# Kernel tuning notes

Hardware: AMD Instinct MI355X
Metric: run time of the kernel (lower is better)

Reference implementation:

```python
import jax, jax.numpy as jnp
import numpy as np

B, H, S, DH = 2, 16, 2048, 64
MASK_FILL = -10000.0


def setup_inputs() -> dict:
    key = jax.random.key(0)
    kq, kk, kv = jax.random.split(key, 3)
    q = jax.random.normal(kq, (B, H, S, DH), dtype=jnp.float32)
    k = jax.random.normal(kk, (B, H, S, DH), dtype=jnp.float32)
    v = jax.random.normal(kv, (B, H, S, DH), dtype=jnp.float32)
    # causal mask: True where attention is disallowed (upper triangle)
    mask = jnp.triu(jnp.ones((S, S), dtype=jnp.bool_), k=1)
    return {"q": q, "k": k, "v": v, "mask": mask}


def reference(q, k, v, mask):
    scale = 1.0 / jnp.sqrt(jnp.asarray(k.shape[-1], dtype=q.dtype))
    # scores: [B, H, S_q, S_k]
    scores = jnp.einsum("bhqd,bhkd->bhqk", q, k) * scale
    # additive mask: masked_fill on a zeros [S_k, S_v] matrix -> -10000 where mask
    attn_bias = jnp.where(mask, jnp.asarray(MASK_FILL, dtype=k.dtype),
                          jnp.asarray(0.0, dtype=k.dtype))
    scores = scores + attn_bias  # broadcast over batch/heads
    attn = jax.nn.softmax(scores, axis=-1)
    # dropout_rate = 0.0 -> identity
    return jnp.einsum("bhqk,bhkd->bhqd", attn, v)
```

## Files before the change

kernel.cpp:

```cpp
#include <hip/hip_runtime.h>


#define S_LEN  2048
#define DHDIM  64
#define NHEADS 32
#define LDP    72
#define M2     23.083120654223414f
#define QSCALE 0.18033688011117658f
#define NSLOT  27

typedef __attribute__((ext_vector_type(8))) short bf16x8;
typedef __attribute__((ext_vector_type(4))) float f32x4;
typedef __attribute__((ext_vector_type(16))) float f32x16;

#define RT(qp,k0,k1,sl) ((unsigned)(qp)<<24 | (unsigned)(k0)<<16 | (unsigned)(k1)<<8 | (unsigned)(sl))
__device__ __constant__ unsigned RTAB32[32] = {
    RT(15,0,11,24),  RT(15,11,22,25), RT(10,0,11,10),  RT(10,11,22,11),
    RT(15,22,32,26), RT(14,0,10,21),  RT(14,10,20,22), RT(14,20,30,23),
    RT(13,0,10,18),  RT(9,0,10,8),    RT(9,10,20,9),   RT(4,0,10,255),
    RT(13,10,19,19), RT(13,19,28,20), RT(12,0,9,15),   RT(12,9,18,16),
    RT(8,0,9,6),     RT(8,9,18,7),    RT(12,18,26,17), RT(11,0,8,12),
    RT(11,8,16,13),  RT(11,16,24,14), RT(7,0,8,4),     RT(7,8,16,5),
    RT(3,0,8,255),   RT(6,0,7,2),     RT(6,7,14,3),    RT(5,0,6,0),
    RT(5,6,12,1),    RT(2,0,6,255),   RT(1,0,4,255),   RT(0,0,2,255)};

__device__ __forceinline__ float fast_exp2(float x) {
#if __has_builtin(__builtin_amdgcn_exp2f)
    return __builtin_amdgcn_exp2f(x);
#else
    return exp2f(x);
#endif
}
__device__ __forceinline__ unsigned short f2bf(float f) {
    unsigned u = __float_as_uint(f);
    return (unsigned short)((u + 0x7fffu + ((u >> 16) & 1u)) >> 16);
}
__device__ __forceinline__ void ld8(const float* p, float* f) {
    float4 a = *(const float4*)p, b = *(const float4*)(p + 4);
    f[0]=a.x; f[1]=a.y; f[2]=a.z; f[3]=a.w; f[4]=b.x; f[5]=b.y; f[6]=b.z; f[7]=b.w;
}
__device__ __forceinline__ uint4 pack8(const float* f, float scale) {
    union { uint4 v; unsigned short s[8]; } w;
    #pragma unroll
    for (int j = 0; j < 8; j++) w.s[j] = f2bf(f[j] * scale);
    return w.v;
}
__device__ __forceinline__ unsigned packhi(float a, float b) {
#if __has_builtin(__builtin_amdgcn_perm)
    return __builtin_amdgcn_perm(__float_as_uint(b), __float_as_uint(a), 0x07060302u);
#else
    return (__float_as_uint(a) >> 16) | (__float_as_uint(b) & 0xffff0000u);
#endif
}
__device__ __forceinline__ bf16x8 mk_bf16x8(unsigned d0, unsigned d1,
                                            unsigned d2, unsigned d3) {
    union { unsigned u[4]; bf16x8 v; } w;
    w.u[0] = d0; w.u[1] = d1; w.u[2] = d2; w.u[3] = d3;
    return w.v;
}

__global__ __launch_bounds__(256) void prep(
    const float* __restrict__ Qf, const float* __restrict__ Kf,
    const float* __restrict__ Vf, unsigned short* __restrict__ qb,
    unsigned short* __restrict__ kb, unsigned short* __restrict__ vtb)
{
    const int st = blockIdx.x, bh = blockIdx.y;
    __shared__ unsigned lt32[64][LDP / 2];
    const float* vp = Vf + ((size_t)bh * S_LEN + st * 64) * DHDIM;
    {
        const int c = threadIdx.x;
        const int sp = c >> 3;
        const int d0 = (c & 7) * 8;
        float fa[8], fb[8];
        ld8(vp + (2 * sp) * DHDIM + d0, fa);
        ld8(vp + (2 * sp + 1) * DHDIM + d0, fb);
        #pragma unroll
        for (int j = 0; j < 8; j++) {
            int d = d0 + j;
            int colw = (sp & 3) | ((((sp >> 2) ^ (d >> 3)) & 7) << 2);
            lt32[d][colw] = (unsigned)f2bf(fa[j]) | ((unsigned)f2bf(fb[j]) << 16);
        }
    }
    size_t off = ((size_t)(bh * 32 + st) * 4096) + (size_t)threadIdx.x * 16;
    float f[8];
    ld8(Qf + off, f);     *(uint4*)(qb + off)     = pack8(f, QSCALE);
    ld8(Qf + off + 8, f); *(uint4*)(qb + off + 8) = pack8(f, QSCALE);
    ld8(Kf + off, f);     *(uint4*)(kb + off)     = pack8(f, 1.0f);
    ld8(Kf + off + 8, f); *(uint4*)(kb + off + 8) = pack8(f, 1.0f);
    __syncthreads();
    unsigned short* op = vtb + (size_t)bh * DHDIM * S_LEN + st * 64;
    for (int c = threadIdx.x; c < 512; c += 256) {
        int d = c >> 3, q = c & 7;
        int colw = ((q ^ (d >> 3)) & 7) << 2;
        *(uint4*)(op + (size_t)d * S_LEN + q * 8) = *(const uint4*)&lt32[d][colw];
    }
}

__global__ __launch_bounds__(512) void fattn_splitk(
    const unsigned short* __restrict__ Qp, const unsigned short* __restrict__ Kp,
    const unsigned short* __restrict__ Vp,
    float* __restrict__ pO, float* __restrict__ pL, float* __restrict__ O)
{
    __shared__ unsigned short smem[256 * LDP];
    unsigned short (*ksA)[LDP]  = (unsigned short(*)[LDP])smem;
    unsigned short (*ksB)[LDP]  = (unsigned short(*)[LDP])(smem + 64 * LDP);
    unsigned short (*vtsA)[LDP] = (unsigned short(*)[LDP])(smem + 128 * LDP);
    unsigned short (*vtsB)[LDP] = (unsigned short(*)[LDP])(smem + 192 * LDP);

    const int bh   = blockIdx.x;
    const unsigned e = RTAB32[blockIdx.y];
    const int qp   = e >> 24;
    const int k0   = (e >> 16) & 255;
    const int k1   = (e >> 8) & 255;
    const int sl   = e & 255;
    const bool whole = (sl == 255);

    const int tid  = threadIdx.x;
    const int wave = tid >> 6, lane = tid & 63;
    const int q31  = lane & 31, hi = lane >> 5;
    const int qh   = wave & 3, kh = wave >> 2;
    const int qrow = qh * 32 + q31;
    const int gq   = qp * 128 + qrow;
    const int diag_kt = gq >> 6;

    const unsigned short* qsrc = Qp + ((size_t)bh * S_LEN + gq) * DHDIM;
    const bf16x8 bq0 = *(const bf16x8*)(qsrc + hi * 8);
    const bf16x8 bq1 = *(const bf16x8*)(qsrc + 16 + hi * 8);
    const bf16x8 bq2 = *(const bf16x8*)(qsrc + 32 + hi * 8);
    const bf16x8 bq3 = *(const bf16x8*)(qsrc + 48 + hi * 8);

    f32x16 of2[2];
    #pragma unroll
    for (int i = 0; i < 16; i++) { of2[0][i] = 0.f; of2[1][i] = 0.f; }
    float l_p = 0.f;

    const unsigned short* Kbh = Kp + (size_t)bh * S_LEN * DHDIM;
    const unsigned short* Vbh = Vp + (size_t)bh * DHDIM * S_LEN;
    const int sr = tid >> 3, sc = (tid & 7) * 8;
    uint4 kr, vr;
    kr = *(const uint4*)(Kbh + ((size_t)k0 * 64 + sr) * DHDIM + sc);
    vr = *(const uint4*)(Vbh + (size_t)sr * S_LEN + k0 * 64 + sc);
    {
        unsigned short (*ks)[LDP]  = (k0 & 1) ? ksB : ksA;
        unsigned short (*vts)[LDP] = (k0 & 1) ? vtsB : vtsA;
        *(uint4*)&ks[sr][sc]  = kr;
        *(uint4*)&vts[sr][sc] = vr;
    }
    if (k0 + 1 < k1) {
        kr = *(const uint4*)(Kbh + ((size_t)(k0 + 1) * 64 + sr) * DHDIM + sc);
        vr = *(const uint4*)(Vbh + (size_t)sr * S_LEN + (k0 + 1) * 64 + sc);
    }

    for (int kt = k0; kt < k1; kt++) {
        __syncthreads();

        if (kt + 1 < k1) {
            unsigned short (*ks)[LDP]  = ((kt + 1) & 1) ? ksB : ksA;
            unsigned short (*vts)[LDP] = ((kt + 1) & 1) ? vtsB : vtsA;
            *(uint4*)&ks[sr][sc]  = kr;
            *(uint4*)&vts[sr][sc] = vr;
            if (kt + 2 < k1) {
                kr = *(const uint4*)(Kbh + ((size_t)(kt + 2) * 64 + sr) * DHDIM + sc);
                vr = *(const uint4*)(Vbh + (size_t)sr * S_LEN + (kt + 2) * 64 + sc);
            }
        }

        if (kt > diag_kt) continue;

        const unsigned short (*ksc)[LDP] = (kt & 1) ? ksB : ksA;
        const unsigned short (*vtc)[LDP] = (kt & 1) ? vtsB : vtsA;

        f32x16 sf;
        #pragma unroll
        for (int i = 0; i < 16; i++) sf[i] = -M2;
        __builtin_amdgcn_s_setprio(1);
        {
            bf16x8 ak = *(const bf16x8*)&ksc[kh * 32 + q31][hi * 8];
            sf = __builtin_amdgcn_mfma_f32_32x32x16_bf16(ak, bq0, sf, 0, 0, 0);
            ak = *(const bf16x8*)&ksc[kh * 32 + q31][16 + hi * 8];
            sf = __builtin_amdgcn_mfma_f32_32x32x16_bf16(ak, bq1, sf, 0, 0, 0);
            ak = *(const bf16x8*)&ksc[kh * 32 + q31][32 + hi * 8];
            sf = __builtin_amdgcn_mfma_f32_32x32x16_bf16(ak, bq2, sf, 0, 0, 0);
            ak = *(const bf16x8*)&ksc[kh * 32 + q31][48 + hi * 8];
            sf = __builtin_amdgcn_mfma_f32_32x32x16_bf16(ak, bq3, sf, 0, 0, 0);
        }
        __builtin_amdgcn_s_setprio(0);

        const bool diag = (kt == diag_kt);
        const int qmod = gq & 63;
        unsigned pdw[8];
        #pragma unroll
        for (int g = 0; g < 4; g++) {
            float p[4];
            #pragma unroll
            for (int r2 = 0; r2 < 4; r2++) {
                float pv = fast_exp2(sf[g * 4 + r2]);
                if (diag) {
                    const int kl = kh * 32 + 8 * g + 4 * hi + r2;
                    if (kl > qmod) pv = 0.f;
                }
                p[r2] = pv;
                l_p += pv;
            }
            pdw[g * 2]     = packhi(p[0], p[1]);
            pdw[g * 2 + 1] = packhi(p[2], p[3]);
        }

        __builtin_amdgcn_s_setprio(1);
        #pragma unroll
        for (int js = 0; js < 2; js++) {
            const unsigned a0 = pdw[4 * js],     a1 = pdw[4 * js + 1];
            const unsigned b0 = pdw[4 * js + 2], b1 = pdw[4 * js + 3];
            const unsigned pa0 = __shfl_xor(a0, 32), pa1 = __shfl_xor(a1, 32);
            const unsigned pb0 = __shfl_xor(b0, 32), pb1 = __shfl_xor(b1, 32);
            const bf16x8 bp = mk_bf16x8(hi ? pb0 : a0, hi ? pb1 : a1,
                                        hi ? b0 : pa0, hi ? b1 : pa1);
            const int scol = (2 * kh + js) * 16 + hi * 8;
            bf16x8 av = *(const bf16x8*)&vtc[q31][scol];
            of2[0] = __builtin_amdgcn_mfma_f32_32x32x16_bf16(av, bp, of2[0], 0, 0, 0);
            av = *(const bf16x8*)&vtc[32 + q31][scol];
            of2[1] = __builtin_amdgcn_mfma_f32_32x32x16_bf16(av, bp, of2[1], 0, 0, 0);
        }
        __builtin_amdgcn_s_setprio(0);
    }

    float l2 = l_p + __shfl_xor(l_p, 32);
    __syncthreads();
    float* fs = (float*)smem;
    const int base = (qh * 64 + lane) * 36;
    if (kh == 1) {
        #pragma unroll
        for (int dh = 0; dh < 2; dh++)
            #pragma unroll
            for (int g = 0; g < 4; g++)
                *(float4*)&fs[base + dh * 16 + g * 4] = make_float4(
                    of2[dh][4 * g], of2[dh][4 * g + 1],
                    of2[dh][4 * g + 2], of2[dh][4 * g + 3]);
        fs[base + 32] = l2;
    }
    __syncthreads();
    if (kh == 0) {
        #pragma unroll
        for (int dh = 0; dh < 2; dh++)
            #pragma unroll
            for (int g = 0; g < 4; g++) {
                float4 a = *(const float4*)&fs[base + dh * 16 + g * 4];
                of2[dh][4 * g]     += a.x;
                of2[dh][4 * g + 1] += a.y;
                of2[dh][4 * g + 2] += a.z;
                of2[dh][4 * g + 3] += a.w;
            }
        l2 += fs[base + 32];

        if (whole) {
            const float inv = 1.f / l2;
            float* op = O + ((size_t)bh * S_LEN + gq) * DHDIM;
            #pragma unroll
            for (int dh = 0; dh < 2; dh++)
                #pragma unroll
                for (int g = 0; g < 4; g++)
                    *(float4*)(op + dh * 32 + 8 * g + 4 * hi) = make_float4(
                        of2[dh][4 * g] * inv, of2[dh][4 * g + 1] * inv,
                        of2[dh][4 * g + 2] * inv, of2[dh][4 * g + 3] * inv);
        } else {
            const int slot = bh * NSLOT + sl;
            if (hi == 0) pL[slot * 128 + qrow] = l2;
            float* op = pO + (size_t)slot * 8192 + qrow * 64;
            #pragma unroll
            for (int dh = 0; dh < 2; dh++)
                #pragma unroll
                for (int g = 0; g < 4; g++)
                    *(float4*)(op + dh * 32 + 8 * g + 4 * hi) = make_float4(
                        of2[dh][4 * g], of2[dh][4 * g + 1],
                        of2[dh][4 * g + 2], of2[dh][4 * g + 3]);
        }
    }
}

__global__ __launch_bounds__(256) void combine(
    const float* __restrict__ pO, const float* __restrict__ pL,
    float* __restrict__ O)
{
    const int t = 5 + blockIdx.x, bh = blockIdx.y;
    int base, cnt;
    if (t <= 10) { base = (t - 5) * 2;       cnt = 2; }
    else         { base = 12 + (t - 11) * 3; cnt = 3; }
    const int sb = bh * NSLOT + base;
    const float* A = pO + (size_t)sb * 8192;
    float* out = O + ((size_t)bh * S_LEN + t * 128) * DHDIM;
    #pragma unroll
    for (int k = 0; k < 8; k++) {
        int c = threadIdx.x + k * 256;
        int row = c >> 4;
        float l = pL[sb * 128 + row] + pL[(sb + 1) * 128 + row];
        float4 a = *(const float4*)(A + c * 4);
        float4 b = *(const float4*)(A + 8192 + c * 4);
        float4 s = make_float4(a.x + b.x, a.y + b.y, a.z + b.z, a.w + b.w);
        if (cnt == 3) {
            l += pL[(sb + 2) * 128 + row];
            float4 d = *(const float4*)(A + 16384 + c * 4);
            s = make_float4(s.x + d.x, s.y + d.y, s.z + d.z, s.w + d.w);
        }
        float inv = 1.f / l;
        *(float4*)(out + c * 4) = make_float4(
            s.x * inv, s.y * inv, s.z * inv, s.w * inv);
    }
}

template <bool PRE>
__global__ __launch_bounds__(256) void fattn_kernel(
    const void* __restrict__ Qp, const void* __restrict__ Kp,
    const void* __restrict__ Vp, float* __restrict__ O)
{
    __shared__ unsigned short smem[192 * LDP];
    unsigned short (*ks)[LDP]  = (unsigned short(*)[LDP])smem;
    unsigned short (*vts)[LDP] = (unsigned short(*)[LDP])(smem + 64 * LDP);
    unsigned short (*qs)[LDP]  = (unsigned short(*)[LDP])(smem + 128 * LDP);
    unsigned short (*pst)[LDP] = qs;

    const int id = blockIdx.y * 32 + blockIdx.x;
    const int g  = id >> 8;
    const int r8 = id & 255;
    const int bh = r8 >> 3;
    const int s8 = r8 & 7;
    const int qt = (g == 0) ? 31 - 2 * s8 : (g == 1) ? 2 * s8
                 : (g == 2) ? 30 - 2 * s8 : 2 * s8 + 1;

    const int tid = threadIdx.x;
    const int wave = tid >> 6, lane = tid & 63;
    const int quad = lane >> 4, l16 = lane & 15;

    if constexpr (PRE) {
        const unsigned short* src = (const unsigned short*)Qp
            + ((size_t)bh * S_LEN + qt * 64) * DHDIM;
        for (int c = tid; c < 512; c += 256) {
            int row = c >> 3, c8 = (c & 7) * 8;
            *(uint4*)&qs[row][c8] = *(const uint4*)(src + row * DHDIM + c8);
        }
    } else {
        const float* src = (const float*)Qp + ((size_t)bh * S_LEN + qt * 64) * DHDIM;
        for (int c = tid; c < 512; c += 256) {
            int row = c >> 3, c8 = (c & 7) * 8;
            float f[8]; ld8(src + row * DHDIM + c8, f);
            *(uint4*)&qs[row][c8] = pack8(f, QSCALE);
        }
    }
    __syncthreads();

    const int prow = wave * 16 + l16;
    const bf16x8 bq0 = *(const bf16x8*)&qs[prow][quad * 8];
    const bf16x8 bq1 = *(const bf16x8*)&qs[prow][32 + quad * 8];

    float l_p = 0.f;
    f32x4 of[4];
    #pragma unroll
    for (int n = 0; n < 4; n++) of[n] = (f32x4){0.f, 0.f, 0.f, 0.f};

    for (int kt = 0; kt <= qt; kt++) {
        __syncthreads();
        if constexpr (PRE) {
            const unsigned short* ksrc = (const unsigned short*)Kp
                + ((size_t)bh * S_LEN + kt * 64) * DHDIM;
            const unsigned short* vsrc = (const unsigned short*)Vp
                + (size_t)bh * DHDIM * S_LEN + kt * 64;
            for (int c = tid; c < 512; c += 256) {
                int row = c >> 3, c8 = (c & 7) * 8;
                *(uint4*)&ks[row][c8]  = *(const uint4*)(ksrc + row * DHDIM + c8);
                *(uint4*)&vts[row][c8] = *(const uint4*)(vsrc + (size_t)row * S_LEN + c8);
            }
        } else {
            const float* ksrc = (const float*)Kp + ((size_t)bh * S_LEN + kt * 64) * DHDIM;
            const float* vsrc = (const float*)Vp + ((size_t)bh * S_LEN + kt * 64) * DHDIM;
            for (int c = tid; c < 512; c += 256) {
                int row = c >> 3, c8 = (c & 7) * 8;
                float f[8];
                ld8(ksrc + row * DHDIM + c8, f);
                *(uint4*)&ks[row][c8] = pack8(f, 1.0f);
                ld8(vsrc + row * DHDIM + c8, f);
                #pragma unroll
                for (int j = 0; j < 8; j++) vts[c8 + j][row] = f2bf(f[j]);
            }
        }
        __syncthreads();

        f32x4 sf[4];
        #pragma unroll
        for (int n = 0; n < 4; n++) {
            bf16x8 ak0 = *(const bf16x8*)&ks[n * 16 + l16][quad * 8];
            bf16x8 ak1 = *(const bf16x8*)&ks[n * 16 + l16][32 + quad * 8];
            sf[n] = (f32x4){-M2, -M2, -M2, -M2};
            sf[n] = __builtin_amdgcn_mfma_f32_16x16x32_bf16(ak0, bq0, sf[n], 0, 0, 0);
            sf[n] = __builtin_amdgcn_mfma_f32_16x16x32_bf16(ak1, bq1, sf[n], 0, 0, 0);
        }

        const bool diag = (kt == qt);
        #pragma unroll
        for (int n = 0; n < 4; n++) {
            float p[4];
            #pragma unroll
            for (int r = 0; r < 4; r++) {
                p[r] = fast_exp2(sf[n][r]);
                if (diag && (n * 16 + quad * 4 + r > prow)) p[r] = 0.f;
                l_p += p[r];
            }
            uint2 dw;
            dw.x = packhi(p[0], p[1]);
            dw.y = packhi(p[2], p[3]);
            *(uint2*)&pst[prow][n * 16 + quad * 4] = dw;
        }
        asm volatile("s_waitcnt lgkmcnt(0)" ::: "memory");

        bf16x8 bp0 = *(const bf16x8*)&pst[prow][quad * 8];
        bf16x8 bp1 = *(const bf16x8*)&pst[prow][32 + quad * 8];
        #pragma unroll
        for (int n = 0; n < 4; n++) {
            bf16x8 av0 = *(const bf16x8*)&vts[n * 16 + l16][quad * 8];
            bf16x8 av1 = *(const bf16x8*)&vts[n * 16 + l16][32 + quad * 8];
            of[n] = __builtin_amdgcn_mfma_f32_16x16x32_bf16(av0, bp0, of[n], 0, 0, 0);
            of[n] = __builtin_amdgcn_mfma_f32_16x16x32_bf16(av1, bp1, of[n], 0, 0, 0);
        }
    }

    l_p += __shfl_xor(l_p, 16);
    l_p += __shfl_xor(l_p, 32);
    const float inv = 1.f / l_p;
    float* op = O + ((size_t)bh * S_LEN + qt * 64 + prow) * DHDIM;
    #pragma unroll
    for (int n = 0; n < 4; n++)
        *(float4*)(op + n * 16 + quad * 4) = make_float4(
            of[n][0] * inv, of[n][1] * inv, of[n][2] * inv, of[n][3] * inv);
}

extern "C" void kernel_launch(void* const* d_in, const int* in_sizes, int n_in,
                              void* d_out, int out_size, void* d_ws, size_t ws_size,
                              hipStream_t stream) {
    const float* Q = (const float*)d_in[0];
    const float* K = (const float*)d_in[1];
    const float* V = (const float*)d_in[2];
    float* O = (float*)d_out;
    const size_t N = (size_t)NHEADS * S_LEN * DHDIM;
    const size_t prepB  = 3 * N * sizeof(unsigned short);
    const size_t partB  = (size_t)NSLOT * 32 * (8192 + 128) * sizeof(float);

    if (d_ws && ws_size >= prepB + partB) {
        unsigned short* qb  = (unsigned short*)d_ws;
        unsigned short* kb  = qb + N;
        unsigned short* vtb = kb + N;
        float* pO = (float*)((char*)d_ws + prepB);
        float* pL = pO + (size_t)NSLOT * 32 * 8192;
        prep<<<dim3(S_LEN / 64, NHEADS), 256, 0, stream>>>(Q, K, V, qb, kb, vtb);
        fattn_splitk<<<dim3(32, 32), 512, 0, stream>>>(qb, kb, vtb, pO, pL, O);
        combine<<<dim3(11, 32), 256, 0, stream>>>(pO, pL, O);
    } else if (d_ws && ws_size >= prepB) {
        unsigned short* qb  = (unsigned short*)d_ws;
        unsigned short* kb  = qb + N;
        unsigned short* vtb = kb + N;
        prep<<<dim3(S_LEN / 64, NHEADS), 256, 0, stream>>>(Q, K, V, qb, kb, vtb);
        fattn_kernel<true><<<dim3(32, 32), 256, 0, stream>>>(qb, kb, vtb, O);
    } else {
        fattn_kernel<false><<<dim3(32, 32), 256, 0, stream>>>(Q, K, V, O);
    }
}
```

Before: 139.0 us.

## Replace split-K attention plus combine with paired causal q-tile blocks

Drops the split-K flash attention kernel, its partial-output workspace and the separate combine kernel. Each of 256 blocks now handles two 128-row query tiles of one head, one long (15-i) and one short (i), so causal work is balanced across blocks without partial sums. This removes the combine launch and the global traffic for partial results. In exchange the grid shrinks from 1024 blocks to 256, which may underfill the GPU's compute units, and each block processes its two tiles one after the other.

```diff
diff --git a/kernel.cpp b/kernel.cpp
--- a/kernel.cpp
+++ b/kernel.cpp
@@ -7,22 +7,10 @@
 #define LDP    72
 #define M2     23.083120654223414f
 #define QSCALE 0.18033688011117658f
-#define NSLOT  27
 
 typedef __attribute__((ext_vector_type(8))) short bf16x8;
 typedef __attribute__((ext_vector_type(4))) float f32x4;
 typedef __attribute__((ext_vector_type(16))) float f32x16;
-
-#define RT(qp,k0,k1,sl) ((unsigned)(qp)<<24 | (unsigned)(k0)<<16 | (unsigned)(k1)<<8 | (unsigned)(sl))
-__device__ __constant__ unsigned RTAB32[32] = {
-    RT(15,0,11,24),  RT(15,11,22,25), RT(10,0,11,10),  RT(10,11,22,11),
-    RT(15,22,32,26), RT(14,0,10,21),  RT(14,10,20,22), RT(14,20,30,23),
-    RT(13,0,10,18),  RT(9,0,10,8),    RT(9,10,20,9),   RT(4,0,10,255),
-    RT(13,10,19,19), RT(13,19,28,20), RT(12,0,9,15),   RT(12,9,18,16),
-    RT(8,0,9,6),     RT(8,9,18,7),    RT(12,18,26,17), RT(11,0,8,12),
-    RT(11,8,16,13),  RT(11,16,24,14), RT(7,0,8,4),     RT(7,8,16,5),
-    RT(3,0,8,255),   RT(6,0,7,2),     RT(6,7,14,3),    RT(5,0,6,0),
-    RT(5,6,12,1),    RT(2,0,6,255),   RT(1,0,4,255),   RT(0,0,2,255)};
 
 __device__ __forceinline__ float fast_exp2(float x) {
 #if __has_builtin(__builtin_amdgcn_exp2f)
@@ -96,10 +84,9 @@
     }
 }
 
-__global__ __launch_bounds__(512) void fattn_splitk(
+__global__ __launch_bounds__(512) void fattn_single(
     const unsigned short* __restrict__ Qp, const unsigned short* __restrict__ Kp,
-    const unsigned short* __restrict__ Vp,
-    float* __restrict__ pO, float* __restrict__ pL, float* __restrict__ O)
+    const unsigned short* __restrict__ Vp, float* __restrict__ O)
 {
     __shared__ unsigned short smem[256 * LDP];
     unsigned short (*ksA)[LDP]  = (unsigned short(*)[LDP])smem;
@@ -107,152 +94,150 @@
     unsigned short (*vtsA)[LDP] = (unsigned short(*)[LDP])(smem + 128 * LDP);
     unsigned short (*vtsB)[LDP] = (unsigned short(*)[LDP])(smem + 192 * LDP);
 
-    const int bh   = blockIdx.x;
-    const unsigned e = RTAB32[blockIdx.y];
-    const int qp   = e >> 24;
-    const int k0   = (e >> 16) & 255;
-    const int k1   = (e >> 8) & 255;
-    const int sl   = e & 255;
-    const bool whole = (sl == 255);
+    const int b  = blockIdx.x;
+    const int bh = b >> 3, i8 = b & 7;
 
     const int tid  = threadIdx.x;
     const int wave = tid >> 6, lane = tid & 63;
     const int q31  = lane & 31, hi = lane >> 5;
     const int qh   = wave & 3, kh = wave >> 2;
     const int qrow = qh * 32 + q31;
-    const int gq   = qp * 128 + qrow;
-    const int diag_kt = gq >> 6;
-
-    const unsigned short* qsrc = Qp + ((size_t)bh * S_LEN + gq) * DHDIM;
-    const bf16x8 bq0 = *(const bf16x8*)(qsrc + hi * 8);
-    const bf16x8 bq1 = *(const bf16x8*)(qsrc + 16 + hi * 8);
-    const bf16x8 bq2 = *(const bf16x8*)(qsrc + 32 + hi * 8);
-    const bf16x8 bq3 = *(const bf16x8*)(qsrc + 48 + hi * 8);
-
-    f32x16 of2[2];
-    #pragma unroll
-    for (int i = 0; i < 16; i++) { of2[0][i] = 0.f; of2[1][i] = 0.f; }
-    float l_p = 0.f;
 
     const unsigned short* Kbh = Kp + (size_t)bh * S_LEN * DHDIM;
     const unsigned short* Vbh = Vp + (size_t)bh * DHDIM * S_LEN;
     const int sr = tid >> 3, sc = (tid & 7) * 8;
-    uint4 kr, vr;
-    kr = *(const uint4*)(Kbh + ((size_t)k0 * 64 + sr) * DHDIM + sc);
-    vr = *(const uint4*)(Vbh + (size_t)sr * S_LEN + k0 * 64 + sc);
-    {
-        unsigned short (*ks)[LDP]  = (k0 & 1) ? ksB : ksA;
-        unsigned short (*vts)[LDP] = (k0 & 1) ? vtsB : vtsA;
-        *(uint4*)&ks[sr][sc]  = kr;
-        *(uint4*)&vts[sr][sc] = vr;
-    }
-    if (k0 + 1 < k1) {
-        kr = *(const uint4*)(Kbh + ((size_t)(k0 + 1) * 64 + sr) * DHDIM + sc);
-        vr = *(const uint4*)(Vbh + (size_t)sr * S_LEN + (k0 + 1) * 64 + sc);
-    }
-
-    for (int kt = k0; kt < k1; kt++) {
-        __syncthreads();
-
-        if (kt + 1 < k1) {
-            unsigned short (*ks)[LDP]  = ((kt + 1) & 1) ? ksB : ksA;
-            unsigned short (*vts)[LDP] = ((kt + 1) & 1) ? vtsB : vtsA;
-            *(uint4*)&ks[sr][sc]  = kr;
-            *(uint4*)&vts[sr][sc] = vr;
-            if (kt + 2 < k1) {
-                kr = *(const uint4*)(Kbh + ((size_t)(kt + 2) * 64 + sr) * DHDIM + sc);
-                vr = *(const uint4*)(Vbh + (size_t)sr * S_LEN + (kt + 2) * 64 + sc);
-            }
-        }
-
-        if (kt > diag_kt) continue;
-
-        const unsigned short (*ksc)[LDP] = (kt & 1) ? ksB : ksA;
-        const unsigned short (*vtc)[LDP] = (kt & 1) ? vtsB : vtsA;
-
-        f32x16 sf;
-        #pragma unroll
-        for (int i = 0; i < 16; i++) sf[i] = -M2;
-        __builtin_amdgcn_s_setprio(1);
-        {
-            bf16x8 ak = *(const bf16x8*)&ksc[kh * 32 + q31][hi * 8];
-            sf = __builtin_amdgcn_mfma_f32_32x32x16_bf16(ak, bq0, sf, 0, 0, 0);
-            ak = *(const bf16x8*)&ksc[kh * 32 + q31][16 + hi * 8];
-            sf = __builtin_amdgcn_mfma_f32_32x32x16_bf16(ak, bq1, sf, 0, 0, 0);
-            ak = *(const bf16x8*)&ksc[kh * 32 + q31][32 + hi * 8];
-            sf = __builtin_amdgcn_mfma_f32_32x32x16_bf16(ak, bq2, sf, 0, 0, 0);
-            ak = *(const bf16x8*)&ksc[kh * 32 + q31][48 + hi * 8];
-            sf = __builtin_amdgcn_mfma_f32_32x32x16_bf16(ak, bq3, sf, 0, 0, 0);
-        }
-        __builtin_amdgcn_s_setprio(0);
-
-        const bool diag = (kt == diag_kt);
-        const int qmod = gq & 63;
-        unsigned pdw[8];
-        #pragma unroll
-        for (int g = 0; g < 4; g++) {
-            float p[4];
-            #pragma unroll
-            for (int r2 = 0; r2 < 4; r2++) {
-                float pv = fast_exp2(sf[g * 4 + r2]);
-                if (diag) {
-                    const int kl = kh * 32 + 8 * g + 4 * hi + r2;
-                    if (kl > qmod) pv = 0.f;
+
+    #pragma unroll 1
+    for (int it = 0; it < 2; ++it) {
+        const int qp = it ? i8 : (15 - i8);
+        const int k1 = 2 * qp + 2;
+        const int gq = qp * 128 + qrow;
+        const int diag_kt = gq >> 6;
+
+        const unsigned short* qsrc = Qp + ((size_t)bh * S_LEN + gq) * DHDIM;
+        const bf16x8 bq0 = *(const bf16x8*)(qsrc + hi * 8);
+        const bf16x8 bq1 = *(const bf16x8*)(qsrc + 16 + hi * 8);
+        const bf16x8 bq2 = *(const bf16x8*)(qsrc + 32 + hi * 8);
+        const bf16x8 bq3 = *(const bf16x8*)(qsrc + 48 + hi * 8);
+
+        f32x16 of2[2];
+        #pragma unroll
+        for (int i = 0; i < 16; i++) { of2[0][i] = 0.f; of2[1][i] = 0.f; }
+        float l_p = 0.f;
+
+        __syncthreads();
+
+        uint4 kr, vr;
+        kr = *(const uint4*)(Kbh + (size_t)sr * DHDIM + sc);
+        vr = *(const uint4*)(Vbh + (size_t)sr * S_LEN + sc);
+        *(uint4*)&ksA[sr][sc]  = kr;
+        *(uint4*)&vtsA[sr][sc] = vr;
+        if (1 < k1) {
+            kr = *(const uint4*)(Kbh + ((size_t)64 + sr) * DHDIM + sc);
+            vr = *(const uint4*)(Vbh + (size_t)sr * S_LEN + 64 + sc);
+        }
+
+        for (int kt = 0; kt < k1; kt++) {
+            __syncthreads();
+
+            if (kt + 1 < k1) {
+                unsigned short (*ks)[LDP]  = ((kt + 1) & 1) ? ksB : ksA;
+                unsigned short (*vts)[LDP] = ((kt + 1) & 1) ? vtsB : vtsA;
+                *(uint4*)&ks[sr][sc]  = kr;
+                *(uint4*)&vts[sr][sc] = vr;
+                if (kt + 2 < k1) {
+                    kr = *(const uint4*)(Kbh + ((size_t)(kt + 2) * 64 + sr) * DHDIM + sc);
+                    vr = *(const uint4*)(Vbh + (size_t)sr * S_LEN + (kt + 2) * 64 + sc);
                 }
-                p[r2] = pv;
-                l_p += pv;
-            }
-            pdw[g * 2]     = packhi(p[0], p[1]);
-            pdw[g * 2 + 1] = packhi(p[2], p[3]);
-        }
-
-        __builtin_amdgcn_s_setprio(1);
-        #pragma unroll
-        for (int js = 0; js < 2; js++) {
-            const unsigned a0 = pdw[4 * js],     a1 = pdw[4 * js + 1];
-            const unsigned b0 = pdw[4 * js + 2], b1 = pdw[4 * js + 3];
-            const unsigned pa0 = __shfl_xor(a0, 32), pa1 = __shfl_xor(a1, 32);
-            const unsigned pb0 = __shfl_xor(b0, 32), pb1 = __shfl_xor(b1, 32);
-            const bf16x8 bp = mk_bf16x8(hi ? pb0 : a0, hi ? pb1 : a1,
-                                        hi ? b0 : pa0, hi ? b1 : pa1);
-            const int scol = (2 * kh + js) * 16 + hi * 8;
-            bf16x8 av = *(const bf16x8*)&vtc[q31][scol];
-            of2[0] = __builtin_amdgcn_mfma_f32_32x32x16_bf16(av, bp, of2[0], 0, 0, 0);
-            av = *(const bf16x8*)&vtc[32 + q31][scol];
-            of2[1] = __builtin_amdgcn_mfma_f32_32x32x16_bf16(av, bp, of2[1], 0, 0, 0);
-        }
-        __builtin_amdgcn_s_setprio(0);
-    }
-
-    float l2 = l_p + __shfl_xor(l_p, 32);
-    __syncthreads();
-    float* fs = (float*)smem;
-    const int base = (qh * 64 + lane) * 36;
-    if (kh == 1) {
-        #pragma unroll
-        for (int dh = 0; dh < 2; dh++)
-            #pragma unroll
-            for (int g = 0; g < 4; g++)
-                *(float4*)&fs[base + dh * 16 + g * 4] = make_float4(
-                    of2[dh][4 * g], of2[dh][4 * g + 1],
-                    of2[dh][4 * g + 2], of2[dh][4 * g + 3]);
-        fs[base + 32] = l2;
-    }
-    __syncthreads();
-    if (kh == 0) {
-        #pragma unroll
-        for (int dh = 0; dh < 2; dh++)
+            }
+
+            if (kt > diag_kt) continue;
+
+            const unsigned short (*ksc)[LDP] = (kt & 1) ? ksB : ksA;
+            const unsigned short (*vtc)[LDP] = (kt & 1) ? vtsB : vtsA;
+
+            f32x16 sf;
+            #pragma unroll
+            for (int i = 0; i < 16; i++) sf[i] = -M2;
+            __builtin_amdgcn_s_setprio(1);
+            {
+                bf16x8 ak = *(const bf16x8*)&ksc[kh * 32 + q31][hi * 8];
+                sf = __builtin_amdgcn_mfma_f32_32x32x16_bf16(ak, bq0, sf, 0, 0, 0);
+                ak = *(const bf16x8*)&ksc[kh * 32 + q31][16 + hi * 8];
+                sf = __builtin_amdgcn_mfma_f32_32x32x16_bf16(ak, bq1, sf, 0, 0, 0);
+                ak = *(const bf16x8*)&ksc[kh * 32 + q31][32 + hi * 8];
+                sf = __builtin_amdgcn_mfma_f32_32x32x16_bf16(ak, bq2, sf, 0, 0, 0);
+                ak = *(const bf16x8*)&ksc[kh * 32 + q31][48 + hi * 8];
+                sf = __builtin_amdgcn_mfma_f32_32x32x16_bf16(ak, bq3, sf, 0, 0, 0);
+            }
+            __builtin_amdgcn_s_setprio(0);
+
+            const bool diag = (kt == diag_kt);
+            const int qmod = gq & 63;
+            unsigned pdw[8];
             #pragma unroll
             for (int g = 0; g < 4; g++) {
-                float4 a = *(const float4*)&fs[base + dh * 16 + g * 4];
-                of2[dh][4 * g]     += a.x;
-                of2[dh][4 * g + 1] += a.y;
-                of2[dh][4 * g + 2] += a.z;
-                of2[dh][4 * g + 3] += a.w;
-            }
-        l2 += fs[base + 32];
-
-        if (whole) {
+                float p[4];
+                #pragma unroll
+                for (int r2 = 0; r2 < 4; r2++) {
+                    float pv = fast_exp2(sf[g * 4 + r2]);
+                    if (diag) {
+                        const int kl = kh * 32 + 8 * g + 4 * hi + r2;
+                        if (kl > qmod) pv = 0.f;
+                    }
+                    p[r2] = pv;
+                    l_p += pv;
+                }
+                pdw[g * 2]     = packhi(p[0], p[1]);
+                pdw[g * 2 + 1] = packhi(p[2], p[3]);
+            }
+
+            __builtin_amdgcn_s_setprio(1);
+            #pragma unroll
+            for (int js = 0; js < 2; js++) {
+                const unsigned a0 = pdw[4 * js],     a1 = pdw[4 * js + 1];
+                const unsigned b0 = pdw[4 * js + 2], b1 = pdw[4 * js + 3];
+                const unsigned pa0 = __shfl_xor(a0, 32), pa1 = __shfl_xor(a1, 32);
+                const unsigned pb0 = __shfl_xor(b0, 32), pb1 = __shfl_xor(b1, 32);
+                const bf16x8 bp = mk_bf16x8(hi ? pb0 : a0, hi ? pb1 : a1,
+                                            hi ? b0 : pa0, hi ? b1 : pa1);
+                const int scol = (2 * kh + js) * 16 + hi * 8;
+                bf16x8 av = *(const bf16x8*)&vtc[q31][scol];
+                of2[0] = __builtin_amdgcn_mfma_f32_32x32x16_bf16(av, bp, of2[0], 0, 0, 0);
+                av = *(const bf16x8*)&vtc[32 + q31][scol];
+                of2[1] = __builtin_amdgcn_mfma_f32_32x32x16_bf16(av, bp, of2[1], 0, 0, 0);
+            }
+            __builtin_amdgcn_s_setprio(0);
+        }
+
+        float l2 = l_p + __shfl_xor(l_p, 32);
+        __syncthreads();
+        float* fs = (float*)smem;
+        const int base = (qh * 64 + lane) * 36;
+        if (kh == 1) {
+            #pragma unroll
+            for (int dh = 0; dh < 2; dh++)
+                #pragma unroll
+                for (int g = 0; g < 4; g++)
+                    *(float4*)&fs[base + dh * 16 + g * 4] = make_float4(
+                        of2[dh][4 * g], of2[dh][4 * g + 1],
+                        of2[dh][4 * g + 2], of2[dh][4 * g + 3]);
+            fs[base + 32] = l2;
+        }
+        __syncthreads();
+        if (kh == 0) {
+            #pragma unroll
+            for (int dh = 0; dh < 2; dh++)
+                #pragma unroll
+                for (int g = 0; g < 4; g++) {
+                    float4 a = *(const float4*)&fs[base + dh * 16 + g * 4];
+                    of2[dh][4 * g]     += a.x;
+                    of2[dh][4 * g + 1] += a.y;
+                    of2[dh][4 * g + 2] += a.z;
+                    of2[dh][4 * g + 3] += a.w;
+                }
+            l2 += fs[base + 32];
+
             const float inv = 1.f / l2;
             float* op = O + ((size_t)bh * S_LEN + gq) * DHDIM;
             #pragma unroll
@@ -262,48 +247,7 @@
                     *(float4*)(op + dh * 32 + 8 * g + 4 * hi) = make_float4(
                         of2[dh][4 * g] * inv, of2[dh][4 * g + 1] * inv,
                         of2[dh][4 * g + 2] * inv, of2[dh][4 * g + 3] * inv);
-        } else {
-            const int slot = bh * NSLOT + sl;
-            if (hi == 0) pL[slot * 128 + qrow] = l2;
-            float* op = pO + (size_t)slot * 8192 + qrow * 64;
-            #pragma unroll
-            for (int dh = 0; dh < 2; dh++)
-                #pragma unroll
-                for (int g = 0; g < 4; g++)
-                    *(float4*)(op + dh * 32 + 8 * g + 4 * hi) = make_float4(
-                        of2[dh][4 * g], of2[dh][4 * g + 1],
-                        of2[dh][4 * g + 2], of2[dh][4 * g + 3]);
-        }
-    }
-}
-
-__global__ __launch_bounds__(256) void combine(
-    const float* __restrict__ pO, const float* __restrict__ pL,
-    float* __restrict__ O)
-{
-    const int t = 5 + blockIdx.x, bh = blockIdx.y;
-    int base, cnt;
-    if (t <= 10) { base = (t - 5) * 2;       cnt = 2; }
-    else         { base = 12 + (t - 11) * 3; cnt = 3; }
-    const int sb = bh * NSLOT + base;
-    const float* A = pO + (size_t)sb * 8192;
-    float* out = O + ((size_t)bh * S_LEN + t * 128) * DHDIM;
-    #pragma unroll
-    for (int k = 0; k < 8; k++) {
-        int c = threadIdx.x + k * 256;
-        int row = c >> 4;
-        float l = pL[sb * 128 + row] + pL[(sb + 1) * 128 + row];
-        float4 a = *(const float4*)(A + c * 4);
-        float4 b = *(const float4*)(A + 8192 + c * 4);
-        float4 s = make_float4(a.x + b.x, a.y + b.y, a.z + b.z, a.w + b.w);
-        if (cnt == 3) {
-            l += pL[(sb + 2) * 128 + row];
-            float4 d = *(const float4*)(A + 16384 + c * 4);
-            s = make_float4(s.x + d.x, s.y + d.y, s.z + d.z, s.w + d.w);
-        }
-        float inv = 1.f / l;
-        *(float4*)(out + c * 4) = make_float4(
-            s.x * inv, s.y * inv, s.z * inv, s.w * inv);
+        }
     }
 }
 
@@ -440,23 +384,13 @@
     float* O = (float*)d_out;
     const size_t N = (size_t)NHEADS * S_LEN * DHDIM;
     const size_t prepB  = 3 * N * sizeof(unsigned short);
-    const size_t partB  = (size_t)NSLOT * 32 * (8192 + 128) * sizeof(float);
-
-    if (d_ws && ws_size >= prepB + partB) {
-        unsigned short* qb  = (unsigned short*)d_ws;
-        unsigned short* kb  = qb + N;
-        unsigned short* vtb = kb + N;
-        float* pO = (float*)((char*)d_ws + prepB);
-        float* pL = pO + (size_t)NSLOT * 32 * 8192;
-        prep<<<dim3(S_LEN / 64, NHEADS), 256, 0, stream>>>(Q, K, V, qb, kb, vtb);
-        fattn_splitk<<<dim3(32, 32), 512, 0, stream>>>(qb, kb, vtb, pO, pL, O);
-        combine<<<dim3(11, 32), 256, 0, stream>>>(pO, pL, O);
-    } else if (d_ws && ws_size >= prepB) {
+
+    if (d_ws && ws_size >= prepB) {
         unsigned short* qb  = (unsigned short*)d_ws;
         unsigned short* kb  = qb + N;
         unsigned short* vtb = kb + N;
         prep<<<dim3(S_LEN / 64, NHEADS), 256, 0, stream>>>(Q, K, V, qb, kb, vtb);
-        fattn_kernel<true><<<dim3(32, 32), 256, 0, stream>>>(qb, kb, vtb, O);
+        fattn_single<<<dim3(256), 512, 0, stream>>>(qb, kb, vtb, O);
     } else {
         fattn_kernel<false><<<dim3(32, 32), 256, 0, stream>>>(Q, K, V, O);
     }
```

Measured after the change: 142.8 us. +2.7%, slower.
